# Kernel tuning notes

Hardware: AMD Instinct MI355X
Metric: run time of the kernel (lower is better)

## Reference

```python
import jax, jax.numpy as jnp
import numpy as np

B, N, FIN, FOUT, N_TASKS = 32, 1024, 1024, 1024, 16

def setup_inputs() -> dict:
    key = jax.random.key(0)
    k1, k2, k3 = jax.random.split(key, 3)
    x = jax.random.normal(k1, (B, N, FIN), dtype=jnp.float32)
    task_id = jax.random.randint(k2, (B,), 0, N_TASKS, dtype=jnp.int64)
    # Embedding table: one flattened [fout*fin] weight matrix per task
    # (kaiming-style scale for 'relu' init, matching get_rnd_weight intent)
    scale = np.sqrt(2.0 / FIN).astype(np.float32)
    W = jax.random.normal(k3, (N_TASKS, FOUT * FIN), dtype=jnp.float32) * scale
    return {"x": x, "task_id": task_id, "W": W}

def reference(x, task_id, W):
    # gather per-sample weight: [B, fout, fin]
    w = W[task_id].reshape(-1, FOUT, FIN)
    # axis == 2: contract over feature dim d=fin
    out = jnp.einsum('bnd,bcd->bnc', x, w)  # [B, N, fout]
    return (out, task_id)
```

## Files before the change

kernel.cpp:

```cpp
#include <hip/hip_runtime.h>

typedef _Float16 f16;
typedef _Float16 f16x8 __attribute__((ext_vector_type(8)));
typedef __fp16   h16x2 __attribute__((ext_vector_type(2)));
typedef float    f32x4 __attribute__((ext_vector_type(4)));

constexpr int NB = 32;
constexpr int NN = 1024;
constexpr int KK = 1024;
constexpr int MO = 1024;
constexpr int BM = 128, BN = 128, BK = 32;
constexpr int LDA = 40;

__global__ __launch_bounds__(256)
void cond_linear_kernel(const float* __restrict__ x,
                        const int* __restrict__ task_id,
                        const float* __restrict__ W,
                        float* __restrict__ out) {
    __shared__ __align__(16) f16 As[BM * LDA];
    __shared__ __align__(16) f16 Bs[BN * LDA];

    const int bid   = blockIdx.x;
    const int batch = bid >> 6;
    const int tile  = bid & 63;
    const int tm    = tile >> 3;
    const int tn    = tile & 7;

    const int tid  = threadIdx.x;
    const int task = task_id[batch];

    const float* xb = x + (size_t)batch * NN * KK + (size_t)(tm * BM) * KK;
    const float* wb = W + (size_t)task * MO * KK + (size_t)(tn * BN) * KK;

    const int c0 = tid, c1 = tid + 256;
    const int r0 = c0 >> 2, ko0 = (c0 & 3) * 8;
    const int r1 = c1 >> 2, ko1 = (c1 & 3) * 8;

    const float* pa0 = xb + r0 * KK + ko0;
    const float* pa1 = xb + r1 * KK + ko1;
    const float* pb0 = wb + r0 * KK + ko0;
    const float* pb1 = wb + r1 * KK + ko1;

    f32x4 ra[4], rb[4];

    auto load_tile = [&](int k0) {
        ra[0] = *(const f32x4*)(pa0 + k0);
        ra[1] = *(const f32x4*)(pa0 + k0 + 4);
        ra[2] = *(const f32x4*)(pa1 + k0);
        ra[3] = *(const f32x4*)(pa1 + k0 + 4);
        rb[0] = *(const f32x4*)(pb0 + k0);
        rb[1] = *(const f32x4*)(pb0 + k0 + 4);
        rb[2] = *(const f32x4*)(pb1 + k0);
        rb[3] = *(const f32x4*)(pb1 + k0 + 4);
    };

    auto cvt8 = [](const f32x4& lo, const f32x4& hi) -> f16x8 {
        union { h16x2 h[4]; f16x8 v; } u;
        u.h[0] = __builtin_amdgcn_cvt_pkrtz(lo[0], lo[1]);
        u.h[1] = __builtin_amdgcn_cvt_pkrtz(lo[2], lo[3]);
        u.h[2] = __builtin_amdgcn_cvt_pkrtz(hi[0], hi[1]);
        u.h[3] = __builtin_amdgcn_cvt_pkrtz(hi[2], hi[3]);
        return u.v;
    };

    auto store_lds = [&]() {
        *(f16x8*)&As[r0 * LDA + ko0] = cvt8(ra[0], ra[1]);
        *(f16x8*)&As[r1 * LDA + ko1] = cvt8(ra[2], ra[3]);
        *(f16x8*)&Bs[r0 * LDA + ko0] = cvt8(rb[0], rb[1]);
        *(f16x8*)&Bs[r1 * LDA + ko1] = cvt8(rb[2], rb[3]);
    };

    const int lane = tid & 63;
    const int wave = tid >> 6;
    const int wr   = (wave >> 1) * 64;
    const int wc   = (wave & 1) * 64;
    const int lm   = lane & 15;
    const int lq   = lane >> 4;

    f32x4 acc[4][4] = {};

    const f16* pAs = &As[(wr + lm) * LDA + lq * 8];
    const f16* pBs = &Bs[(wc + lm) * LDA + lq * 8];

    load_tile(0);
    for (int ks = 0; ks < KK / BK; ++ks) {
        store_lds();
        __syncthreads();
        if (ks + 1 < KK / BK) load_tile((ks + 1) * BK);

        f16x8 af[4], bf[4];
        #pragma unroll
        for (int i = 0; i < 4; ++i) af[i] = *(const f16x8*)(pAs + i * 16 * LDA);
        #pragma unroll
        for (int j = 0; j < 4; ++j) bf[j] = *(const f16x8*)(pBs + j * 16 * LDA);

        #pragma unroll
        for (int i = 0; i < 4; ++i)
            #pragma unroll
            for (int j = 0; j < 4; ++j)
                acc[i][j] = __builtin_amdgcn_mfma_f32_16x16x32_f16(af[i], bf[j], acc[i][j], 0, 0, 0);

        __syncthreads();
    }

    float* ob = out + (size_t)batch * NN * MO + (size_t)(tm * BM) * MO + (tn * BN);
    #pragma unroll
    for (int i = 0; i < 4; ++i) {
        #pragma unroll
        for (int j = 0; j < 4; ++j) {
            const int row0 = wr + i * 16 + lq * 4;
            const int col  = wc + j * 16 + lm;
            #pragma unroll
            for (int r = 0; r < 4; ++r)
                ob[(size_t)(row0 + r) * MO + col] = acc[i][j][r];
        }
    }

    if (tile == 0 && tid == 0)
        out[(size_t)NB * NN * MO + batch] = (float)task;
}

extern "C" void kernel_launch(void* const* d_in, const int* in_sizes, int n_in,
                              void* d_out, int out_size, void* d_ws, size_t ws_size,
                              hipStream_t stream) {
    const float* x       = (const float*)d_in[0];
    const int*   task_id = (const int*)d_in[1];
    const float* W       = (const float*)d_in[2];
    float*       out     = (float*)d_out;

    dim3 grid(NB * (NN / BM) * (MO / BN));
    dim3 block(256);
    cond_linear_kernel<<<grid, block, 0, stream>>>(x, task_id, W, out);
}
```

Measured before the change: 378.7 us.

## Double-buffer LDS tiles with two-deep register prefetch and swap tile order

Shared-memory tiles become double-buffered and two register sets prefetch global loads two K-steps ahead. This halves the number of barriers per K step and overlaps global loads and LDS stores with MFMA work. The tile index mapping is also swapped so that consecutive blocks share the same weight column tile, and launch bounds now request two blocks per CU. In exchange the kernel uses more registers and twice the LDS, which may limit occupancy.

```diff
diff --git a/kernel.cpp b/kernel.cpp
--- a/kernel.cpp
+++ b/kernel.cpp
@@ -5,26 +5,24 @@
 typedef __fp16   h16x2 __attribute__((ext_vector_type(2)));
 typedef float    f32x4 __attribute__((ext_vector_type(4)));
 
-constexpr int NB = 32;
-constexpr int NN = 1024;
-constexpr int KK = 1024;
-constexpr int MO = 1024;
+constexpr int NB = 32, NN = 1024, KK = 1024, MO = 1024;
 constexpr int BM = 128, BN = 128, BK = 32;
 constexpr int LDA = 40;
+constexpr int NSTEP = KK / BK;
 
-__global__ __launch_bounds__(256)
+__global__ __launch_bounds__(256, 2)
 void cond_linear_kernel(const float* __restrict__ x,
                         const int* __restrict__ task_id,
                         const float* __restrict__ W,
                         float* __restrict__ out) {
-    __shared__ __align__(16) f16 As[BM * LDA];
-    __shared__ __align__(16) f16 Bs[BN * LDA];
+    __shared__ __align__(16) f16 As[2][BM * LDA];
+    __shared__ __align__(16) f16 Bs[2][BN * LDA];
 
     const int bid   = blockIdx.x;
     const int batch = bid >> 6;
     const int tile  = bid & 63;
-    const int tm    = tile >> 3;
-    const int tn    = tile & 7;
+    const int tm = tile & 7;
+    const int tn = tile >> 3;
 
     const int tid  = threadIdx.x;
     const int task = task_id[batch];
@@ -41,17 +39,19 @@
     const float* pb0 = wb + r0 * KK + ko0;
     const float* pb1 = wb + r1 * KK + ko1;
 
-    f32x4 ra[4], rb[4];
+    f32x4 ra0[4], rb0[4], ra1[4], rb1[4];
 
-    auto load_tile = [&](int k0) {
-        ra[0] = *(const f32x4*)(pa0 + k0);
-        ra[1] = *(const f32x4*)(pa0 + k0 + 4);
-        ra[2] = *(const f32x4*)(pa1 + k0);
-        ra[3] = *(const f32x4*)(pa1 + k0 + 4);
-        rb[0] = *(const f32x4*)(pb0 + k0);
-        rb[1] = *(const f32x4*)(pb0 + k0 + 4);
-        rb[2] = *(const f32x4*)(pb1 + k0);
-        rb[3] = *(const f32x4*)(pb1 + k0 + 4);
+    auto load0 = [&](int k0) {
+        ra0[0] = *(const f32x4*)(pa0 + k0); ra0[1] = *(const f32x4*)(pa0 + k0 + 4);
+        ra0[2] = *(const f32x4*)(pa1 + k0); ra0[3] = *(const f32x4*)(pa1 + k0 + 4);
+        rb0[0] = *(const f32x4*)(pb0 + k0); rb0[1] = *(const f32x4*)(pb0 + k0 + 4);
+        rb0[2] = *(const f32x4*)(pb1 + k0); rb0[3] = *(const f32x4*)(pb1 + k0 + 4);
+    };
+    auto load1 = [&](int k0) {
+        ra1[0] = *(const f32x4*)(pa0 + k0); ra1[1] = *(const f32x4*)(pa0 + k0 + 4);
+        ra1[2] = *(const f32x4*)(pa1 + k0); ra1[3] = *(const f32x4*)(pa1 + k0 + 4);
+        rb1[0] = *(const f32x4*)(pb0 + k0); rb1[1] = *(const f32x4*)(pb0 + k0 + 4);
+        rb1[2] = *(const f32x4*)(pb1 + k0); rb1[3] = *(const f32x4*)(pb1 + k0 + 4);
     };
 
     auto cvt8 = [](const f32x4& lo, const f32x4& hi) -> f16x8 {
@@ -63,11 +63,17 @@
         return u.v;
     };
 
-    auto store_lds = [&]() {
-        *(f16x8*)&As[r0 * LDA + ko0] = cvt8(ra[0], ra[1]);
-        *(f16x8*)&As[r1 * LDA + ko1] = cvt8(ra[2], ra[3]);
-        *(f16x8*)&Bs[r0 * LDA + ko0] = cvt8(rb[0], rb[1]);
-        *(f16x8*)&Bs[r1 * LDA + ko1] = cvt8(rb[2], rb[3]);
+    auto store0 = [&](int buf) {
+        *(f16x8*)&As[buf][r0 * LDA + ko0] = cvt8(ra0[0], ra0[1]);
+        *(f16x8*)&As[buf][r1 * LDA + ko1] = cvt8(ra0[2], ra0[3]);
+        *(f16x8*)&Bs[buf][r0 * LDA + ko0] = cvt8(rb0[0], rb0[1]);
+        *(f16x8*)&Bs[buf][r1 * LDA + ko1] = cvt8(rb0[2], rb0[3]);
+    };
+    auto store1 = [&](int buf) {
+        *(f16x8*)&As[buf][r0 * LDA + ko0] = cvt8(ra1[0], ra1[1]);
+        *(f16x8*)&As[buf][r1 * LDA + ko1] = cvt8(ra1[2], ra1[3]);
+        *(f16x8*)&Bs[buf][r0 * LDA + ko0] = cvt8(rb1[0], rb1[1]);
+        *(f16x8*)&Bs[buf][r1 * LDA + ko1] = cvt8(rb1[2], rb1[3]);
     };
 
     const int lane = tid & 63;
@@ -79,27 +85,35 @@
 
     f32x4 acc[4][4] = {};
 
-    const f16* pAs = &As[(wr + lm) * LDA + lq * 8];
-    const f16* pBs = &Bs[(wc + lm) * LDA + lq * 8];
+    const int fa_off = (wr + lm) * LDA + lq * 8;
+    const int fb_off = (wc + lm) * LDA + lq * 8;
 
-    load_tile(0);
-    for (int ks = 0; ks < KK / BK; ++ks) {
-        store_lds();
-        __syncthreads();
-        if (ks + 1 < KK / BK) load_tile((ks + 1) * BK);
-
+    auto compute = [&](int buf) {
         f16x8 af[4], bf[4];
         #pragma unroll
-        for (int i = 0; i < 4; ++i) af[i] = *(const f16x8*)(pAs + i * 16 * LDA);
+        for (int i = 0; i < 4; ++i) af[i] = *(const f16x8*)&As[buf][fa_off + i * 16 * LDA];
         #pragma unroll
-        for (int j = 0; j < 4; ++j) bf[j] = *(const f16x8*)(pBs + j * 16 * LDA);
-
+        for (int j = 0; j < 4; ++j) bf[j] = *(const f16x8*)&Bs[buf][fb_off + j * 16 * LDA];
         #pragma unroll
         for (int i = 0; i < 4; ++i)
             #pragma unroll
             for (int j = 0; j < 4; ++j)
                 acc[i][j] = __builtin_amdgcn_mfma_f32_16x16x32_f16(af[i], bf[j], acc[i][j], 0, 0, 0);
+    };
 
+    load0(0);
+    load1(BK);
+    store0(0);
+    __syncthreads();
+
+    for (int ks = 0; ks < NSTEP; ks += 2) {
+        if (ks + 2 < NSTEP) load0((ks + 2) * BK);
+        compute(0);
+        store1(1);
+        __syncthreads();
+        if (ks + 3 < NSTEP) load1((ks + 3) * BK);
+        compute(1);
+        if (ks + 2 < NSTEP) store0(0);
         __syncthreads();
     }
 
```

After: 372.2 us. About the same (-1.7%).
